# Kernel tuning notes

Hardware: AMD Instinct MI355X
Metric: run time of the kernel (lower is better)

Reference implementation:

```python
import jax, jax.numpy as jnp
import numpy as np

N_EMBD = 1024
N_HEAD = 16
DIM_HEAD = N_EMBD // N_HEAD
SCALE = DIM_HEAD ** (-0.5)  # source divides by this (i.e. multiplies scores by sqrt(dim_head))


def setup_inputs() -> dict:
    key = jax.random.key(0)
    k1, k2, k3, k4, k5 = jax.random.split(key, 5)
    B, Tq, Tkv = 2, 2048, 2048
    x_q = jax.random.normal(k1, (B, Tq, N_EMBD), dtype=jnp.float32)
    x_kv = jax.random.normal(k2, (B, Tkv, N_EMBD), dtype=jnp.float32)
    s = 0.02
    W_q = jax.random.normal(k3, (N_EMBD, N_EMBD), dtype=jnp.float32) * s
    W_kv = jax.random.normal(k4, (N_EMBD, 2 * N_EMBD), dtype=jnp.float32) * s
    W_proj = jax.random.normal(k5, (N_EMBD, N_EMBD), dtype=jnp.float32) * s
    return {"x_q": x_q, "x_kv": x_kv, "W_q": W_q, "W_kv": W_kv, "W_proj": W_proj}


def reference(x_q, x_kv, W_q, W_kv, W_proj):
    B, Tq, C = x_q.shape
    Tkv = x_kv.shape[1]
    q = x_q @ W_q                      # [B, Tq, C]
    kv = x_kv @ W_kv                   # [B, Tkv, 2C]
    k, v = jnp.split(kv, 2, axis=2)
    # [B, H, T, Dh]
    q = q.reshape(B, Tq, N_HEAD, DIM_HEAD).transpose(0, 2, 1, 3)
    k = k.reshape(B, Tkv, N_HEAD, DIM_HEAD).transpose(0, 2, 1, 3)
    v = v.reshape(B, Tkv, N_HEAD, DIM_HEAD).transpose(0, 2, 1, 3)
    # Faithful to source: scores = q@k^T / scale  (== * sqrt(dim_head))
    attn = jnp.einsum('bhqd,bhkd->bhqk', q, k) / SCALE
    attn = jax.nn.softmax(attn, axis=-1)
    y = jnp.einsum('bhqk,bhkd->bhqd', attn, v)
    y = y.transpose(0, 2, 1, 3).reshape(B, Tq, C)
    return y @ W_proj
```

## Files before the change

### kernel.cpp

```cpp
#include <hip/hip_runtime.h>
#include <cstddef>

typedef _Float16 f16;
typedef _Float16 f16x8 __attribute__((ext_vector_type(8)));
typedef _Float16 f16x4 __attribute__((ext_vector_type(4)));
typedef _Float16 f16x2 __attribute__((ext_vector_type(2)));
typedef float f32x4 __attribute__((ext_vector_type(4)));
typedef float f32x16 __attribute__((ext_vector_type(16)));
typedef unsigned int u32;

__device__ inline float exp2_fast(float x) {
  float r;
  asm("v_exp_f32 %0, %1" : "=v"(r) : "v"(x));
  return r;
}

__device__ inline void gl_lds16(const f16* g, f16* l) {
  __builtin_amdgcn_global_load_lds(
      (const __attribute__((address_space(1))) u32*)g,
      (__attribute__((address_space(3))) u32*)l, 16, 0, 0);
}

__global__ __launch_bounds__(256) void cvt2_f32_f16(
    const float* __restrict__ a, const float* __restrict__ b,
    f16* __restrict__ oa, f16* __restrict__ ob) {
  int bid = blockIdx.x;
  const float* in;
  f16* out;
  if (bid < 4096) { in = a; out = oa; } else { in = b; out = ob; bid -= 4096; }
  int i = (bid * 256 + threadIdx.x) * 4;
  float4 v = *(const float4*)&in[i];
  f16x4 h;
  h[0] = (f16)v.x; h[1] = (f16)v.y; h[2] = (f16)v.z; h[3] = (f16)v.w;
  *(f16x4*)&out[i] = h;
}

__global__ __launch_bounds__(256) void transpose3(
    const float* __restrict__ Wq, const float* __restrict__ Wkv,
    const float* __restrict__ Wp, f16* __restrict__ Wqt,
    f16* __restrict__ Wkvt, f16* __restrict__ Wpt) {
  __shared__ float t[32][33];
  int z = blockIdx.z;
  const float* in;
  f16* out;
  int N = 1024, extra = 0;
  if (z == 0) { in = Wq; out = Wqt; }
  else if (z == 3) { in = Wp; out = Wpt; }
  else { in = Wkv; out = Wkvt; N = 2048; extra = (z - 1) * 1024; }
  int tx = threadIdx.x % 32, ty = threadIdx.x / 32;
  int n0 = blockIdx.x * 32 + extra, k0 = blockIdx.y * 32;
#pragma unroll
  for (int i = 0; i < 32; i += 8)
    t[ty + i][tx] = in[(size_t)(k0 + ty + i) * N + n0 + tx];
  __syncthreads();
#pragma unroll
  for (int i = 0; i < 32; i += 8)
    out[(size_t)(n0 + ty + i) * 1024 + k0 + tx] = (f16)t[tx][ty + i];
}

template <int BN, typename CT>
__device__ __forceinline__ void gemm_body(
    const f16* __restrict__ A, const f16* __restrict__ Bt, CT* __restrict__ C,
    int bid, int M, int N, int K, float scale, f16* As, f16* Bs) {
  constexpr int NT = BN / 32;
  constexpr int BI = BN / 32;
  const int nb = N / BN;
  const int m0 = (bid / nb) * 128;
  const int n0 = (bid % nb) * BN;
  const int tid = threadIdx.x;
  const int w = tid >> 6, lane = tid & 63;
  const int l16 = lane & 15, quad = lane >> 4;
  const int wrow = (w >> 1) * 64, wcol = (w & 1) * (BN / 2);
  const int sr = tid >> 3, sc = (tid & 7) << 3;

  f32x4 acc[4][NT] = {};

  for (int k0 = 0; k0 < K; k0 += 64) {
#pragma unroll
    for (int i = 0; i < 4; i++)
      gl_lds16(&A[(size_t)(m0 + sr + i * 32) * K + k0 + sc],
               &As[i * 2048 + w * 512]);
#pragma unroll
    for (int i = 0; i < BI; i++)
      gl_lds16(&Bt[(size_t)(n0 + sr + i * 32) * K + k0 + sc],
               &Bs[i * 2048 + w * 512]);
    __syncthreads();

    f16x8 af[4][2], bf[NT][2];
#pragma unroll
    for (int mt = 0; mt < 4; mt++)
#pragma unroll
      for (int s = 0; s < 2; s++)
        af[mt][s] = *(const f16x8*)&As[(wrow + mt * 16 + l16) * 64 + s * 32 + quad * 8];
#pragma unroll
    for (int nt = 0; nt < NT; nt++)
#pragma unroll
      for (int s = 0; s < 2; s++)
        bf[nt][s] = *(const f16x8*)&Bs[(wcol + nt * 16 + l16) * 64 + s * 32 + quad * 8];

#pragma unroll
    for (int mt = 0; mt < 4; mt++)
#pragma unroll
      for (int nt = 0; nt < NT; nt++) {
        acc[mt][nt] = __builtin_amdgcn_mfma_f32_16x16x32_f16(af[mt][0], bf[nt][0], acc[mt][nt], 0, 0, 0);
        acc[mt][nt] = __builtin_amdgcn_mfma_f32_16x16x32_f16(af[mt][1], bf[nt][1], acc[mt][nt], 0, 0, 0);
      }
    __syncthreads();
  }

#pragma unroll
  for (int mt = 0; mt < 4; mt++)
#pragma unroll
    for (int nt = 0; nt < NT; nt++)
#pragma unroll
      for (int r = 0; r < 4; r++) {
        int row = m0 + wrow + mt * 16 + quad * 4 + r;
        int col = n0 + wcol + nt * 16 + l16;
        C[(size_t)row * N + col] = (CT)(acc[mt][nt][r] * scale);
      }
}

__global__ __launch_bounds__(256) void qkv_gemm(
    const f16* __restrict__ Xq, const f16* __restrict__ Wqt, f16* __restrict__ Qh,
    const f16* __restrict__ Xkv, const f16* __restrict__ Wkvt, f16* __restrict__ KVh,
    float sc_q) {
  __shared__ f16 As[128 * 64];
  __shared__ f16 Bs[128 * 64];
  if (blockIdx.x < 256)
    gemm_body<128, f16>(Xq, Wqt, Qh, blockIdx.x, 4096, 1024, 1024, sc_q, As, Bs);
  else
    gemm_body<128, f16>(Xkv, Wkvt, KVh, blockIdx.x - 256, 4096, 2048, 1024, 1.0f, As, Bs);
}

template <int BN, typename CT>
__global__ __launch_bounds__(256) void gemm_lds(
    const f16* __restrict__ A, const f16* __restrict__ Bt, CT* __restrict__ C,
    int M, int N, int K, float scale) {
  __shared__ f16 As[128 * 64];
  __shared__ f16 Bs[BN * 64];
  gemm_body<BN, CT>(A, Bt, C, blockIdx.x, M, N, K, scale, As, Bs);
}

__global__ __launch_bounds__(256) void attn_kernel(
    const f16* __restrict__ Qh, const f16* __restrict__ KVh, f16* __restrict__ Yh) {
  __shared__ f16 smem[18432];
  f16* Ks = smem;
  f16* Vt = smem + 64 * 72;
  f16* Ps = smem + 2 * 64 * 72;

  const int bid = blockIdx.x;
  const int hb = bid & 31;
  const int qt = bid >> 5;
  const int h = hb >> 1, b = hb & 1;
  const int tid = threadIdx.x;
  const int w = tid >> 6, lane = tid & 63;
  const int l31 = lane & 31, e = lane >> 5;

  const size_t qrow0 = (size_t)b * 2048 + (size_t)qt * 128;
  const size_t kvrow0 = (size_t)b * 2048;
  f16* Psw = Ps + w * 32 * 72;

  f16x8 qf[4];
#pragma unroll
  for (int ks = 0; ks < 4; ks++)
    qf[ks] = *(const f16x8*)&Qh[(qrow0 + w * 32 + l31) * 1024 + h * 64 + ks * 16 + e * 8];

  float m_run = -1e30f, l_run = 0.0f;
  f32x16 o_acc[2] = {};

  const int ksr = tid >> 2, ksc = (tid & 3) << 4;
  const int vkv0 = (tid >> 3) * 2;
  const int vd0 = (tid & 7) * 8;
  const int vcol = ((((vkv0 >> 3) ^ (tid & 7)) << 3) | (vkv0 & 7));

  f16x8 kr0, kr1, vr0, vr1;
  {
    const f16* kb = &KVh[(kvrow0 + ksr) * 2048 + h * 64 + ksc];
    kr0 = *(const f16x8*)kb;
    kr1 = *(const f16x8*)(kb + 8);
    const f16* vb = &KVh[(kvrow0 + vkv0) * 2048 + 1024 + h * 64 + vd0];
    vr0 = *(const f16x8*)vb;
    vr1 = *(const f16x8*)(vb + 2048);
  }

  for (int t = 0; t < 32; t++) {
    *(f16x8*)&Ks[ksr * 72 + ksc] = kr0;
    *(f16x8*)&Ks[ksr * 72 + ksc + 8] = kr1;
#pragma unroll
    for (int j = 0; j < 8; j++) {
      f16x2 p; p[0] = vr0[j]; p[1] = vr1[j];
      *(f16x2*)&Vt[(vd0 + j) * 72 + vcol] = p;
    }
    __syncthreads();

    if (t + 1 < 32) {
      const f16* kb = &KVh[(kvrow0 + (t + 1) * 64 + ksr) * 2048 + h * 64 + ksc];
      kr0 = *(const f16x8*)kb;
      kr1 = *(const f16x8*)(kb + 8);
      const f16* vb = &KVh[(kvrow0 + (t + 1) * 64 + vkv0) * 2048 + 1024 + h * 64 + vd0];
      vr0 = *(const f16x8*)vb;
      vr1 = *(const f16x8*)(vb + 2048);
    }

    f32x16 sacc[2] = {};
#pragma unroll
    for (int kvt = 0; kvt < 2; kvt++)
#pragma unroll
      for (int ks = 0; ks < 4; ks++) {
        f16x8 a = *(const f16x8*)&Ks[(kvt * 32 + l31) * 72 + ks * 16 + e * 8];
        sacc[kvt] = __builtin_amdgcn_mfma_f32_32x32x16_f16(a, qf[ks], sacc[kvt], 0, 0, 0);
      }

    float mx = sacc[0][0];
#pragma unroll
    for (int r = 1; r < 16; r++) mx = fmaxf(mx, sacc[0][r]);
#pragma unroll
    for (int r = 0; r < 16; r++) mx = fmaxf(mx, sacc[1][r]);
    mx = fmaxf(mx, __shfl_xor(mx, 32, 64));
    float mnew = fmaxf(m_run, mx);
    float alpha = exp2_fast(m_run - mnew);
    m_run = mnew;

    float ssum = 0.0f;
#pragma unroll
    for (int kvt = 0; kvt < 2; kvt++)
#pragma unroll
      for (int r = 0; r < 16; r++) {
        float p = exp2_fast(sacc[kvt][r] - mnew);
        sacc[kvt][r] = p;
        ssum += p;
      }
    ssum += __shfl_xor(ssum, 32, 64);
    l_run = l_run * alpha + ssum;
#pragma unroll
    for (int r = 0; r < 16; r++) { o_acc[0][r] *= alpha; o_acc[1][r] *= alpha; }

#pragma unroll
    for (int kvt = 0; kvt < 2; kvt++)
#pragma unroll
      for (int r2 = 0; r2 < 4; r2++) {
        f16x4 hh;
        hh[0] = (f16)sacc[kvt][r2 * 4 + 0];
        hh[1] = (f16)sacc[kvt][r2 * 4 + 1];
        hh[2] = (f16)sacc[kvt][r2 * 4 + 2];
        hh[3] = (f16)sacc[kvt][r2 * 4 + 3];
        *(f16x4*)&Psw[l31 * 72 + kvt * 32 + r2 * 8 + e * 4] = hh;
      }

    f16x8 pf[4];
#pragma unroll
    for (int ks = 0; ks < 4; ks++)
      pf[ks] = *(const f16x8*)&Psw[l31 * 72 + ks * 16 + e * 8];
#pragma unroll
    for (int dt = 0; dt < 2; dt++) {
      const int d = dt * 32 + l31;
      const int dx = d >> 3;
#pragma unroll
      for (int ks = 0; ks < 4; ks++) {
        f16x8 va = *(const f16x8*)&Vt[d * 72 + (((ks * 2 + e) ^ dx) << 3)];
        o_acc[dt] = __builtin_amdgcn_mfma_f32_32x32x16_f16(va, pf[ks], o_acc[dt], 0, 0, 0);
      }
    }
    __syncthreads();
  }

  float linv = 1.0f / l_run;
  float* Of = (float*)smem + w * 2176;
#pragma unroll
  for (int dt = 0; dt < 2; dt++)
#pragma unroll
    for (int r2 = 0; r2 < 4; r2++) {
      f32x4 vv;
      vv[0] = o_acc[dt][r2 * 4 + 0] * linv;
      vv[1] = o_acc[dt][r2 * 4 + 1] * linv;
      vv[2] = o_acc[dt][r2 * 4 + 2] * linv;
      vv[3] = o_acc[dt][r2 * 4 + 3] * linv;
      *(f32x4*)&Of[l31 * 68 + dt * 32 + r2 * 8 + e * 4] = vv;
    }
  const int qq = lane >> 1, dh = (lane & 1) * 32;
#pragma unroll
  for (int j = 0; j < 8; j++) {
    f32x4 v = *(const f32x4*)&Of[qq * 68 + dh + j * 4];
    f16x4 hh;
    hh[0] = (f16)v[0]; hh[1] = (f16)v[1]; hh[2] = (f16)v[2]; hh[3] = (f16)v[3];
    *(f16x4*)&Yh[(qrow0 + w * 32 + qq) * 1024 + h * 64 + dh + j * 4] = hh;
  }
}

extern "C" void kernel_launch(void* const* d_in, const int* in_sizes, int n_in,
                              void* d_out, int out_size, void* d_ws, size_t ws_size,
                              hipStream_t stream) {
  const float* x_q  = (const float*)d_in[0];
  const float* x_kv = (const float*)d_in[1];
  const float* W_q  = (const float*)d_in[2];
  const float* W_kv = (const float*)d_in[3];
  const float* W_p  = (const float*)d_in[4];
  float* out = (float*)d_out;

  f16* Wq_t  = (f16*)d_ws;
  f16* Wkv_t = Wq_t  + (size_t)1024 * 1024;
  f16* Wp_t  = Wkv_t + (size_t)2048 * 1024;
  f16* Qh    = Wp_t  + (size_t)1024 * 1024;
  f16* KVh   = Qh    + (size_t)4096 * 1024;
  f16* Yh    = KVh   + (size_t)4096 * 2048;
  f16* Xq_h  = Yh;
  f16* Xkv_h = Yh    + (size_t)4096 * 1024;

  cvt2_f32_f16<<<8192, 256, 0, stream>>>(x_q, x_kv, Xq_h, Xkv_h);
  transpose3<<<dim3(32, 32, 4), 256, 0, stream>>>(W_q, W_kv, W_p, Wq_t, Wkv_t, Wp_t);

  const float SC = 11.5415603f;
  qkv_gemm<<<768, 256, 0, stream>>>(Xq_h, Wq_t, Qh, Xkv_h, Wkv_t, KVh, SC);

  attn_kernel<<<512, 256, 0, stream>>>(Qh, KVh, Yh);

  gemm_lds<64, float><<<512, 256, 0, stream>>>(Yh, Wp_t, out, 4096, 1024, 1024, 1.0f);
}
```

Baseline: 224.7 us.

## Register-prefetch GEMM tiles with XOR-swizzled LDS and merge prep kernels

The GEMM main loop no longer uses direct global-to-LDS loads. It now prefetches the next K tile into registers while the current tile is computed, and stores tiles into LDS with an XOR swizzle so fragment reads avoid bank conflicts. The input conversion and weight transpose kernels are merged into one launch to save a kernel launch, and occupancy hints are added to launch_bounds. The trade-off is higher register pressure, plus a single LDS buffer that still needs two barriers per iteration.

```diff
diff --git a/kernel.cpp b/kernel.cpp
--- a/kernel.cpp
+++ b/kernel.cpp
@@ -15,47 +15,41 @@
   return r;
 }
 
-__device__ inline void gl_lds16(const f16* g, f16* l) {
-  __builtin_amdgcn_global_load_lds(
-      (const __attribute__((address_space(1))) u32*)g,
-      (__attribute__((address_space(3))) u32*)l, 16, 0, 0);
-}
-
-__global__ __launch_bounds__(256) void cvt2_f32_f16(
-    const float* __restrict__ a, const float* __restrict__ b,
-    f16* __restrict__ oa, f16* __restrict__ ob) {
-  int bid = blockIdx.x;
-  const float* in;
-  f16* out;
-  if (bid < 4096) { in = a; out = oa; } else { in = b; out = ob; bid -= 4096; }
-  int i = (bid * 256 + threadIdx.x) * 4;
-  float4 v = *(const float4*)&in[i];
-  f16x4 h;
-  h[0] = (f16)v.x; h[1] = (f16)v.y; h[2] = (f16)v.z; h[3] = (f16)v.w;
-  *(f16x4*)&out[i] = h;
-}
-
-__global__ __launch_bounds__(256) void transpose3(
+__global__ __launch_bounds__(256) void prep(
+    const float* __restrict__ xq, const float* __restrict__ xkv,
+    f16* __restrict__ oq, f16* __restrict__ okv,
     const float* __restrict__ Wq, const float* __restrict__ Wkv,
     const float* __restrict__ Wp, f16* __restrict__ Wqt,
     f16* __restrict__ Wkvt, f16* __restrict__ Wpt) {
   __shared__ float t[32][33];
-  int z = blockIdx.z;
-  const float* in;
-  f16* out;
-  int N = 1024, extra = 0;
-  if (z == 0) { in = Wq; out = Wqt; }
-  else if (z == 3) { in = Wp; out = Wpt; }
-  else { in = Wkv; out = Wkvt; N = 2048; extra = (z - 1) * 1024; }
-  int tx = threadIdx.x % 32, ty = threadIdx.x / 32;
-  int n0 = blockIdx.x * 32 + extra, k0 = blockIdx.y * 32;
-#pragma unroll
-  for (int i = 0; i < 32; i += 8)
-    t[ty + i][tx] = in[(size_t)(k0 + ty + i) * N + n0 + tx];
-  __syncthreads();
-#pragma unroll
-  for (int i = 0; i < 32; i += 8)
-    out[(size_t)(n0 + ty + i) * 1024 + k0 + tx] = (f16)t[tx][ty + i];
+  int bid = blockIdx.x;
+  if (bid < 8192) {
+    const float* in = (bid < 4096) ? xq : xkv;
+    f16* out = (bid < 4096) ? oq : okv;
+    int i = ((bid & 4095) * 256 + threadIdx.x) * 4;
+    float4 v = *(const float4*)&in[i];
+    f16x4 h;
+    h[0] = (f16)v.x; h[1] = (f16)v.y; h[2] = (f16)v.z; h[3] = (f16)v.w;
+    *(f16x4*)&out[i] = h;
+  } else {
+    int zz = bid - 8192;
+    int bx = zz & 31, by = (zz >> 5) & 31, z = zz >> 10;
+    const float* in;
+    f16* out;
+    int N = 1024, extra = 0;
+    if (z == 0) { in = Wq; out = Wqt; }
+    else if (z == 3) { in = Wp; out = Wpt; }
+    else { in = Wkv; out = Wkvt; N = 2048; extra = (z - 1) * 1024; }
+    int tx = threadIdx.x % 32, ty = threadIdx.x / 32;
+    int n0 = bx * 32 + extra, k0 = by * 32;
+#pragma unroll
+    for (int i = 0; i < 32; i += 8)
+      t[ty + i][tx] = in[(size_t)(k0 + ty + i) * N + n0 + tx];
+    __syncthreads();
+#pragma unroll
+    for (int i = 0; i < 32; i += 8)
+      out[(size_t)(n0 + ty + i) * 1024 + k0 + tx] = (f16)t[tx][ty + i];
+  }
 }
 
 template <int BN, typename CT>
@@ -71,40 +65,56 @@
   const int w = tid >> 6, lane = tid & 63;
   const int l16 = lane & 15, quad = lane >> 4;
   const int wrow = (w >> 1) * 64, wcol = (w & 1) * (BN / 2);
-  const int sr = tid >> 3, sc = (tid & 7) << 3;
+  const int sr = tid >> 3, sc8 = tid & 7;
+  const int wc8 = sc8 ^ (sr & 7);
 
   f32x4 acc[4][NT] = {};
+  f16x8 ar[4], br[BI];
+
+#pragma unroll
+  for (int i = 0; i < 4; i++)
+    ar[i] = *(const f16x8*)&A[(size_t)(m0 + sr + i * 32) * K + sc8 * 8];
+#pragma unroll
+  for (int i = 0; i < BI; i++)
+    br[i] = *(const f16x8*)&Bt[(size_t)(n0 + sr + i * 32) * K + sc8 * 8];
 
   for (int k0 = 0; k0 < K; k0 += 64) {
 #pragma unroll
     for (int i = 0; i < 4; i++)
-      gl_lds16(&A[(size_t)(m0 + sr + i * 32) * K + k0 + sc],
-               &As[i * 2048 + w * 512]);
+      *(f16x8*)&As[(sr + i * 32) * 64 + wc8 * 8] = ar[i];
 #pragma unroll
     for (int i = 0; i < BI; i++)
-      gl_lds16(&Bt[(size_t)(n0 + sr + i * 32) * K + k0 + sc],
-               &Bs[i * 2048 + w * 512]);
-    __syncthreads();
-
-    f16x8 af[4][2], bf[NT][2];
-#pragma unroll
-    for (int mt = 0; mt < 4; mt++)
+      *(f16x8*)&Bs[(sr + i * 32) * 64 + wc8 * 8] = br[i];
+    __syncthreads();
+
+    if (k0 + 64 < K) {
+#pragma unroll
+      for (int i = 0; i < 4; i++)
+        ar[i] = *(const f16x8*)&A[(size_t)(m0 + sr + i * 32) * K + k0 + 64 + sc8 * 8];
+#pragma unroll
+      for (int i = 0; i < BI; i++)
+        br[i] = *(const f16x8*)&Bt[(size_t)(n0 + sr + i * 32) * K + k0 + 64 + sc8 * 8];
+    }
+
+    f16x8 bf[NT][2];
+#pragma unroll
+    for (int nt = 0; nt < NT; nt++) {
+      const int row = wcol + nt * 16 + l16;
 #pragma unroll
       for (int s = 0; s < 2; s++)
-        af[mt][s] = *(const f16x8*)&As[(wrow + mt * 16 + l16) * 64 + s * 32 + quad * 8];
-#pragma unroll
-    for (int nt = 0; nt < NT; nt++)
-#pragma unroll
-      for (int s = 0; s < 2; s++)
-        bf[nt][s] = *(const f16x8*)&Bs[(wcol + nt * 16 + l16) * 64 + s * 32 + quad * 8];
-
-#pragma unroll
-    for (int mt = 0; mt < 4; mt++)
+        bf[nt][s] = *(const f16x8*)&Bs[row * 64 + (((s * 4 + quad) ^ (row & 7)) << 3)];
+    }
+#pragma unroll
+    for (int mt = 0; mt < 4; mt++) {
+      const int row = wrow + mt * 16 + l16;
+      f16x8 af0 = *(const f16x8*)&As[row * 64 + ((quad ^ (row & 7)) << 3)];
+      f16x8 af1 = *(const f16x8*)&As[row * 64 + (((4 + quad) ^ (row & 7)) << 3)];
 #pragma unroll
       for (int nt = 0; nt < NT; nt++) {
-        acc[mt][nt] = __builtin_amdgcn_mfma_f32_16x16x32_f16(af[mt][0], bf[nt][0], acc[mt][nt], 0, 0, 0);
-        acc[mt][nt] = __builtin_amdgcn_mfma_f32_16x16x32_f16(af[mt][1], bf[nt][1], acc[mt][nt], 0, 0, 0);
-      }
+        acc[mt][nt] = __builtin_amdgcn_mfma_f32_16x16x32_f16(af0, bf[nt][0], acc[mt][nt], 0, 0, 0);
+        acc[mt][nt] = __builtin_amdgcn_mfma_f32_16x16x32_f16(af1, bf[nt][1], acc[mt][nt], 0, 0, 0);
+      }
+    }
     __syncthreads();
   }
 
@@ -120,7 +130,7 @@
       }
 }
 
-__global__ __launch_bounds__(256) void qkv_gemm(
+__global__ __launch_bounds__(256, 3) void qkv_gemm(
     const f16* __restrict__ Xq, const f16* __restrict__ Wqt, f16* __restrict__ Qh,
     const f16* __restrict__ Xkv, const f16* __restrict__ Wkvt, f16* __restrict__ KVh,
     float sc_q) {
@@ -133,7 +143,7 @@
 }
 
 template <int BN, typename CT>
-__global__ __launch_bounds__(256) void gemm_lds(
+__global__ __launch_bounds__(256, 2) void gemm_lds(
     const f16* __restrict__ A, const f16* __restrict__ Bt, CT* __restrict__ C,
     int M, int N, int K, float scale) {
   __shared__ f16 As[128 * 64];
@@ -306,8 +316,8 @@
   f16* Xq_h  = Yh;
   f16* Xkv_h = Yh    + (size_t)4096 * 1024;
 
-  cvt2_f32_f16<<<8192, 256, 0, stream>>>(x_q, x_kv, Xq_h, Xkv_h);
-  transpose3<<<dim3(32, 32, 4), 256, 0, stream>>>(W_q, W_kv, W_p, Wq_t, Wkv_t, Wp_t);
+  prep<<<12288, 256, 0, stream>>>(x_q, x_kv, Xq_h, Xkv_h,
+                                  W_q, W_kv, W_p, Wq_t, Wkv_t, Wp_t);
 
   const float SC = 11.5415603f;
   qkv_gemm<<<768, 256, 0, stream>>>(Xq_h, Wq_t, Qh, Xkv_h, Wkv_t, KVh, SC);
```

After: 212.0 us. -5.6%, faster.
